# Kernel optimization log

Measured on AMD Instinct MI355X. Metric: run time of the kernel, lower is better.

## Reference

```python
import jax, jax.numpy as jnp
import numpy as np

# Grouped masked GEMM dims (see DeepSeekMOE._up_gate/_down):
# G = num_experts // ep = 8; M = m_per_group = 32
# up/gate: k = hidden_size = 4096, n = 2*expert_dim = 2816
# down   : k = expert_dim  = 1408, n = hidden_size = 4096
G, M = 8, 32
K_UG, N_UG = 4096, 2816
K_DN, N_DN = 1408, 4096


def setup_inputs() -> dict:
    key = jax.random.key(0)
    k1, k2, k3, k4, k5 = jax.random.split(key, 5)
    x_ug = jax.random.normal(k1, (G, M, K_UG), dtype=jnp.float32)
    w_ug = jax.random.normal(k2, (G, N_UG, K_UG), dtype=jnp.float32) * 0.02  # NT layout [g, n, k]
    x_dn = jax.random.normal(k3, (G, M, K_DN), dtype=jnp.float32)
    w_dn = jax.random.normal(k4, (G, N_DN, K_DN), dtype=jnp.float32) * 0.02  # NT layout [g, n, k]
    masked_m = jax.random.randint(k5, (G,), 0, M, dtype=jnp.int32)  # per-group valid row count
    return {"x_ug": x_ug, "w_ug": w_ug, "x_dn": x_dn, "w_dn": w_dn, "masked_m": masked_m}


def reference(x_ug, w_ug, x_dn, w_dn, masked_m):
    # Row-validity mask: rows >= masked_m[g] are skipped by the masked grouped GEMM
    # (their output is zero / undefined; we define it as zero).
    row = jnp.arange(M, dtype=jnp.int32)
    mask = (row[None, :] < masked_m[:, None])[:, :, None]  # [G, M, 1]

    # Masked grouped GEMM, NT layout: out[g] = x[g] @ w[g].T on valid rows.
    out_ug = jnp.einsum('gmk,gnk->gmn', x_ug, w_ug)  # [G, M, N_UG]  up/gate proj
    out_dn = jnp.einsum('gmk,gnk->gmn', x_dn, w_dn)  # [G, M, N_DN]  down proj

    out_ug = jnp.where(mask, out_ug, jnp.zeros((), out_ug.dtype))
    out_dn = jnp.where(mask, out_dn, jnp.zeros((), out_dn.dtype))
    # Pack both grouped-GEMM outputs into one array along the feature dim.
    return jnp.concatenate([out_ug, out_dn], axis=-1)  # [G, M, N_UG + N_DN]
```

## Files before the change

kernel.cpp:

```cpp
#include <hip/hip_runtime.h>
#include <hip/hip_bf16.h>


#define G_    8
#define M_    32
#define KUG   4096
#define NUG   2816
#define KDN   1408
#define NDN   4096
#define NOUT  (NUG + NDN)
#define UPT   (NUG / 32)
#define DNT   (NDN / 32)
#define UPG   (UPT + DNT)
#define BK    128

typedef __attribute__((ext_vector_type(8))) short bf16x8;
typedef __attribute__((ext_vector_type(4))) float f32x4;

typedef __attribute__((address_space(3))) float        lds_f32;
typedef const __attribute__((address_space(1))) float  gbl_f32;

__device__ __forceinline__ short f2bf(float x) {
  union { __hip_bfloat16 h; short s; } u;
  u.h = __hip_bfloat16(x);
  return u.s;
}

__device__ __forceinline__ bf16x8 cvt8(f32x4 lo, f32x4 hi) {
  bf16x8 o;
#pragma unroll
  for (int j = 0; j < 4; ++j) { o[j] = f2bf(lo[j]); o[4 + j] = f2bf(hi[j]); }
  return o;
}

__global__ __launch_bounds__(64, 2) void moe_masked_gemm(
    const float* __restrict__ x_ug, const float* __restrict__ w_ug,
    const float* __restrict__ x_dn, const float* __restrict__ w_dn,
    const int* __restrict__ masked_m, float* __restrict__ out) {
  __shared__ float wbuf[32 * BK];

  int b = blockIdx.x;
  int g = b & 7;
  int u = b >> 3;

  const float* wg;
  const float* xg;
  int K, NIT, n0, colOff;
  if (u < UPT) {
    K = KUG; NIT = KUG / BK; n0 = u * 32; colOff = 0;
    wg = w_ug + ((size_t)g * NUG + n0) * KUG;
    xg = x_ug + (size_t)g * M_ * KUG;
  } else {
    int ud = u - UPT;
    K = KDN; NIT = KDN / BK; n0 = ud * 32; colOff = NUG;
    wg = w_dn + ((size_t)g * NDN + n0) * KDN;
    xg = x_dn + (size_t)g * M_ * KDN;
  }

  int mm = masked_m[g];
  int t   = threadIdx.x;
  int r   = t & 15, q4 = t >> 4;
  int l5  = t >> 5, q32 = t & 31;
  int s   = r & 7;

  f32x4 acc00 = {0.f, 0.f, 0.f, 0.f}, acc01 = {0.f, 0.f, 0.f, 0.f};
  f32x4 acc10 = {0.f, 0.f, 0.f, 0.f}, acc11 = {0.f, 0.f, 0.f, 0.f};

  if (mm != 0) {
    for (int it = 0; it < NIT; ++it) {
      int k0 = it * BK;

#pragma unroll
      for (int i = 0; i < 16; ++i) {
        int row = 2 * i + l5;
        int qs  = q32 ^ (row & 7);
        __builtin_amdgcn_global_load_lds(
            (gbl_f32*)(wg + (size_t)row * K + k0 + qs * 4),
            (lds_f32*)(wbuf + i * 256 + t * 4), 16, 0, 0);
      }

      f32x4 xv[2][4][2];
#pragma unroll
      for (int mf = 0; mf < 2; ++mf) {
#pragma unroll
        for (int ks = 0; ks < 4; ++ks) {
          const float* xp = xg + (size_t)(mf * 16 + r) * K + k0 + ks * 32 + q4 * 8;
          xv[mf][ks][0] = *(const f32x4*)xp;
          xv[mf][ks][1] = *(const f32x4*)(xp + 4);
        }
      }

      asm volatile("s_waitcnt vmcnt(0)" ::: "memory");
      __builtin_amdgcn_sched_barrier(0);

#pragma unroll
      for (int ks = 0; ks < 4; ++ks) {
        int g0 = (ks * 4 + q4) * 2;
        const float* row0 = wbuf + (size_t)r * BK;
        const float* row1 = wbuf + (size_t)(16 + r) * BK;
        f32x4 w0a = *(const f32x4*)(row0 + (((g0)     ^ s) << 2));
        f32x4 w0b = *(const f32x4*)(row0 + (((g0 + 1) ^ s) << 2));
        f32x4 w1a = *(const f32x4*)(row1 + (((g0)     ^ s) << 2));
        f32x4 w1b = *(const f32x4*)(row1 + (((g0 + 1) ^ s) << 2));
        bf16x8 b0 = cvt8(w0a, w0b);
        bf16x8 b1 = cvt8(w1a, w1b);
        bf16x8 a0 = cvt8(xv[0][ks][0], xv[0][ks][1]);
        bf16x8 a1 = cvt8(xv[1][ks][0], xv[1][ks][1]);
        acc00 = __builtin_amdgcn_mfma_f32_16x16x32_bf16(a0, b0, acc00, 0, 0, 0);
        acc01 = __builtin_amdgcn_mfma_f32_16x16x32_bf16(a0, b1, acc01, 0, 0, 0);
        acc10 = __builtin_amdgcn_mfma_f32_16x16x32_bf16(a1, b0, acc10, 0, 0, 0);
        acc11 = __builtin_amdgcn_mfma_f32_16x16x32_bf16(a1, b1, acc11, 0, 0, 0);
      }
    }
  }

  float* outg = out + (size_t)g * M_ * NOUT + colOff + n0;
#pragma unroll
  for (int i = 0; i < 4; ++i) {
    int m0 = q4 * 4 + i;
    int m1 = 16 + m0;
    outg[(size_t)m0 * NOUT + r]      = (m0 < mm) ? acc00[i] : 0.f;
    outg[(size_t)m0 * NOUT + 16 + r] = (m0 < mm) ? acc01[i] : 0.f;
    outg[(size_t)m1 * NOUT + r]      = (m1 < mm) ? acc10[i] : 0.f;
    outg[(size_t)m1 * NOUT + 16 + r] = (m1 < mm) ? acc11[i] : 0.f;
  }
}

extern "C" void kernel_launch(void* const* d_in, const int* in_sizes, int n_in,
                              void* d_out, int out_size, void* d_ws, size_t ws_size,
                              hipStream_t stream) {
  const float* x_ug     = (const float*)d_in[0];
  const float* w_ug     = (const float*)d_in[1];
  const float* x_dn     = (const float*)d_in[2];
  const float* w_dn     = (const float*)d_in[3];
  const int*   masked_m = (const int*)d_in[4];
  float*       out      = (float*)d_out;

  moe_masked_gemm<<<dim3(G_ * UPG), dim3(64), 0, stream>>>(
      x_ug, w_ug, x_dn, w_dn, masked_m, out);
}
```

Before: 122.9 us.

## Split weight staging into two 16-row halves, use larger BK for up-proj, interleave block order

The weight tile is now staged in two 16-row halves, each computed right after it lands, so the same LDS buffer is reused. The up/gate projection uses a 256-wide K step while the down projection keeps 128, which halves the up-proj loop iteration count. Block indices are remapped so each period of 27 blocks mixes 11 up and 16 down tiles, spreading the long and short blocks evenly over the CUs. The cost is an extra serialized vmcnt wait per iteration between the halves, so there is less load/compute overlap inside a block.

```diff
diff --git a/kernel.cpp b/kernel.cpp
--- a/kernel.cpp
+++ b/kernel.cpp
@@ -12,7 +12,6 @@
 #define UPT   (NUG / 32)
 #define DNT   (NDN / 32)
 #define UPG   (UPT + DNT)
-#define BK    128
 
 typedef __attribute__((ext_vector_type(8))) short bf16x8;
 typedef __attribute__((ext_vector_type(4))) float f32x4;
@@ -33,85 +32,117 @@
   return o;
 }
 
+template<int BK>
+__device__ __forceinline__ void stage16(const float* wrows, float* wbuf,
+                                        int K, int k0, int t) {
+  constexpr int GPR = BK / 4;
+  constexpr int NI  = 16 * GPR / 64;
+#pragma unroll
+  for (int i = 0; i < NI; ++i) {
+    int gid = i * 64 + t;
+    int row = gid / GPR;
+    int q   = gid % GPR;
+    int qs  = q ^ (row & 7);
+    __builtin_amdgcn_global_load_lds(
+        (gbl_f32*)(wrows + (size_t)row * K + k0 + qs * 4),
+        (lds_f32*)(wbuf + gid * 4), 16, 0, 0);
+  }
+}
+
+template<int NKS>
+__device__ __forceinline__ void comp16(const float* wbuf, const bf16x8 (&xb)[2][NKS],
+                                       int r, int q4, int s,
+                                       f32x4& accM0, f32x4& accM1) {
+  constexpr int BK = NKS * 32;
+#pragma unroll
+  for (int ks = 0; ks < NKS; ++ks) {
+    int g0 = (ks * 4 + q4) * 2;
+    const float* rowp = wbuf + (size_t)r * BK;
+    f32x4 wlo = *(const f32x4*)(rowp + (((g0)     ^ s) << 2));
+    f32x4 whi = *(const f32x4*)(rowp + (((g0 + 1) ^ s) << 2));
+    bf16x8 bb = cvt8(wlo, whi);
+    accM0 = __builtin_amdgcn_mfma_f32_16x16x32_bf16(xb[0][ks], bb, accM0, 0, 0, 0);
+    accM1 = __builtin_amdgcn_mfma_f32_16x16x32_bf16(xb[1][ks], bb, accM1, 0, 0, 0);
+  }
+}
+
+template<int NKS, int NIT>
+__device__ __forceinline__ void run_unit(const float* wg, const float* xg,
+                                         float* wbuf, int K, int t,
+                                         f32x4& acc00, f32x4& acc01,
+                                         f32x4& acc10, f32x4& acc11) {
+  constexpr int BK = NKS * 32;
+  int r = t & 15, q4 = t >> 4, s = r & 7;
+  for (int it = 0; it < NIT; ++it) {
+    int k0 = it * BK;
+
+    stage16<BK>(wg, wbuf, K, k0, t);
+    f32x4 xv[2][NKS][2];
+#pragma unroll
+    for (int mf = 0; mf < 2; ++mf)
+#pragma unroll
+      for (int ks = 0; ks < NKS; ++ks) {
+        const float* xp = xg + (size_t)(mf * 16 + r) * K + k0 + ks * 32 + q4 * 8;
+        xv[mf][ks][0] = *(const f32x4*)xp;
+        xv[mf][ks][1] = *(const f32x4*)(xp + 4);
+      }
+    asm volatile("s_waitcnt vmcnt(0)" ::: "memory");
+    __builtin_amdgcn_sched_barrier(0);
+
+    bf16x8 xb[2][NKS];
+#pragma unroll
+    for (int mf = 0; mf < 2; ++mf)
+#pragma unroll
+      for (int ks = 0; ks < NKS; ++ks)
+        xb[mf][ks] = cvt8(xv[mf][ks][0], xv[mf][ks][1]);
+
+    comp16<NKS>(wbuf, xb, r, q4, s, acc00, acc10);
+
+    stage16<BK>(wg + (size_t)16 * K, wbuf, K, k0, t);
+    asm volatile("s_waitcnt vmcnt(0)" ::: "memory");
+    __builtin_amdgcn_sched_barrier(0);
+
+    comp16<NKS>(wbuf, xb, r, q4, s, acc01, acc11);
+  }
+}
+
 __global__ __launch_bounds__(64, 2) void moe_masked_gemm(
     const float* __restrict__ x_ug, const float* __restrict__ w_ug,
     const float* __restrict__ x_dn, const float* __restrict__ w_dn,
     const int* __restrict__ masked_m, float* __restrict__ out) {
-  __shared__ float wbuf[32 * BK];
+  __shared__ float wbuf[16 * 256];
 
   int b = blockIdx.x;
   int g = b & 7;
-  int u = b >> 3;
+  int v = b >> 3;
+  int period = v / 27, slot = v - period * 27;
+  int u = (slot < 11) ? (period * 11 + slot) : (UPT + period * 16 + (slot - 11));
 
   const float* wg;
   const float* xg;
-  int K, NIT, n0, colOff;
-  if (u < UPT) {
-    K = KUG; NIT = KUG / BK; n0 = u * 32; colOff = 0;
+  int K, n0, colOff;
+  bool is_up = (u < UPT);
+  if (is_up) {
+    K = KUG; n0 = u * 32; colOff = 0;
     wg = w_ug + ((size_t)g * NUG + n0) * KUG;
     xg = x_ug + (size_t)g * M_ * KUG;
   } else {
     int ud = u - UPT;
-    K = KDN; NIT = KDN / BK; n0 = ud * 32; colOff = NUG;
+    K = KDN; n0 = ud * 32; colOff = NUG;
     wg = w_dn + ((size_t)g * NDN + n0) * KDN;
     xg = x_dn + (size_t)g * M_ * KDN;
   }
 
   int mm = masked_m[g];
-  int t   = threadIdx.x;
-  int r   = t & 15, q4 = t >> 4;
-  int l5  = t >> 5, q32 = t & 31;
-  int s   = r & 7;
+  int t  = threadIdx.x;
+  int r  = t & 15, q4 = t >> 4;
 
   f32x4 acc00 = {0.f, 0.f, 0.f, 0.f}, acc01 = {0.f, 0.f, 0.f, 0.f};
   f32x4 acc10 = {0.f, 0.f, 0.f, 0.f}, acc11 = {0.f, 0.f, 0.f, 0.f};
 
   if (mm != 0) {
-    for (int it = 0; it < NIT; ++it) {
-      int k0 = it * BK;
-
-#pragma unroll
-      for (int i = 0; i < 16; ++i) {
-        int row = 2 * i + l5;
-        int qs  = q32 ^ (row & 7);
-        __builtin_amdgcn_global_load_lds(
-            (gbl_f32*)(wg + (size_t)row * K + k0 + qs * 4),
-            (lds_f32*)(wbuf + i * 256 + t * 4), 16, 0, 0);
-      }
-
-      f32x4 xv[2][4][2];
-#pragma unroll
-      for (int mf = 0; mf < 2; ++mf) {
-#pragma unroll
-        for (int ks = 0; ks < 4; ++ks) {
-          const float* xp = xg + (size_t)(mf * 16 + r) * K + k0 + ks * 32 + q4 * 8;
-          xv[mf][ks][0] = *(const f32x4*)xp;
-          xv[mf][ks][1] = *(const f32x4*)(xp + 4);
-        }
-      }
-
-      asm volatile("s_waitcnt vmcnt(0)" ::: "memory");
-      __builtin_amdgcn_sched_barrier(0);
-
-#pragma unroll
-      for (int ks = 0; ks < 4; ++ks) {
-        int g0 = (ks * 4 + q4) * 2;
-        const float* row0 = wbuf + (size_t)r * BK;
-        const float* row1 = wbuf + (size_t)(16 + r) * BK;
-        f32x4 w0a = *(const f32x4*)(row0 + (((g0)     ^ s) << 2));
-        f32x4 w0b = *(const f32x4*)(row0 + (((g0 + 1) ^ s) << 2));
-        f32x4 w1a = *(const f32x4*)(row1 + (((g0)     ^ s) << 2));
-        f32x4 w1b = *(const f32x4*)(row1 + (((g0 + 1) ^ s) << 2));
-        bf16x8 b0 = cvt8(w0a, w0b);
-        bf16x8 b1 = cvt8(w1a, w1b);
-        bf16x8 a0 = cvt8(xv[0][ks][0], xv[0][ks][1]);
-        bf16x8 a1 = cvt8(xv[1][ks][0], xv[1][ks][1]);
-        acc00 = __builtin_amdgcn_mfma_f32_16x16x32_bf16(a0, b0, acc00, 0, 0, 0);
-        acc01 = __builtin_amdgcn_mfma_f32_16x16x32_bf16(a0, b1, acc01, 0, 0, 0);
-        acc10 = __builtin_amdgcn_mfma_f32_16x16x32_bf16(a1, b0, acc10, 0, 0, 0);
-        acc11 = __builtin_amdgcn_mfma_f32_16x16x32_bf16(a1, b1, acc11, 0, 0, 0);
-      }
-    }
+    if (is_up) run_unit<8, KUG / 256>(wg, xg, wbuf, K, t, acc00, acc01, acc10, acc11);
+    else       run_unit<4, KDN / 128>(wg, xg, wbuf, K, t, acc00, acc01, acc10, acc11);
   }
 
   float* outg = out + (size_t)g * M_ * NOUT + colOff + n0;
```

New measurement: 142.5 us. 1.16x slower.

## Widen N tile to 64, pre-convert activations to bf16, interleave up/down blocks

Applied to the files above, without the earlier changes.

Doubles the per-block N tile from 32 to 64 columns so each activation fragment feeds four MFMA column tiles, halving the activation reloads per weight column. Adds two small pre-pass kernels that convert x_ug and x_dn to bf16 in workspace, so the GEMM reads half the activation bytes and skips per-iteration conversion. Reorders the block index so up and down tiles are interleaved in an 11:16 ratio to balance their differing K lengths across the grid. The cost is fewer blocks (half the grid), a doubled LDS tile that may lower occupancy, and two extra launches.

```diff
diff --git a/kernel.cpp b/kernel.cpp
--- a/kernel.cpp
+++ b/kernel.cpp
@@ -9,10 +9,14 @@
 #define KDN   1408
 #define NDN   4096
 #define NOUT  (NUG + NDN)
-#define UPT   (NUG / 32)
-#define DNT   (NDN / 32)
+#define BN    64
+#define BK    128
+#define UPT   (NUG / BN)
+#define DNT   (NDN / BN)
 #define UPG   (UPT + DNT)
-#define BK    128
+#define XUG_E (G_ * M_ * KUG)
+#define XDN_E (G_ * M_ * KDN)
+#define XBF_BYTES ((size_t)(XUG_E + XDN_E) * 2)
 
 typedef __attribute__((ext_vector_type(8))) short bf16x8;
 typedef __attribute__((ext_vector_type(4))) float f32x4;
@@ -33,61 +37,91 @@
   return o;
 }
 
+__global__ void cvt_x_kernel(const float* __restrict__ src, short* __restrict__ dst,
+                             int n8) {
+  int i = blockIdx.x * 256 + threadIdx.x;
+  if (i < n8) {
+    f32x4 lo = *(const f32x4*)(src + (size_t)i * 8);
+    f32x4 hi = *(const f32x4*)(src + (size_t)i * 8 + 4);
+    *(bf16x8*)(dst + (size_t)i * 8) = cvt8(lo, hi);
+  }
+}
+
+template<bool XBF>
 __global__ __launch_bounds__(64, 2) void moe_masked_gemm(
     const float* __restrict__ x_ug, const float* __restrict__ w_ug,
     const float* __restrict__ x_dn, const float* __restrict__ w_dn,
+    const short* __restrict__ xbf_ug, const short* __restrict__ xbf_dn,
     const int* __restrict__ masked_m, float* __restrict__ out) {
-  __shared__ float wbuf[32 * BK];
+  __shared__ float wbuf[BN * BK];
 
   int b = blockIdx.x;
   int g = b & 7;
-  int u = b >> 3;
+  int v = b >> 3;
+  int p = v / 27, s = v - p * 27;
+  int ub = (s * 11 + 16) / 27;
+  bool is_up = ((s * 11) % 27) < 11;
 
   const float* wg;
-  const float* xg;
-  int K, NIT, n0, colOff;
-  if (u < UPT) {
-    K = KUG; NIT = KUG / BK; n0 = u * 32; colOff = 0;
+  const float* xf;
+  const short* xq;
+  int K, n0, colOff, NIT;
+  if (is_up) {
+    int u = p * 11 + ub;
+    K = KUG; NIT = KUG / BK; n0 = u * BN; colOff = 0;
     wg = w_ug + ((size_t)g * NUG + n0) * KUG;
-    xg = x_ug + (size_t)g * M_ * KUG;
+    xf = x_ug + (size_t)g * M_ * KUG;
+    xq = xbf_ug + (size_t)g * M_ * KUG;
   } else {
-    int ud = u - UPT;
-    K = KDN; NIT = KDN / BK; n0 = ud * 32; colOff = NUG;
+    int d = p * 16 + (s - ub);
+    K = KDN; NIT = KDN / BK; n0 = d * BN; colOff = NUG;
     wg = w_dn + ((size_t)g * NDN + n0) * KDN;
-    xg = x_dn + (size_t)g * M_ * KDN;
+    xf = x_dn + (size_t)g * M_ * KDN;
+    xq = xbf_dn + (size_t)g * M_ * KDN;
   }
 
   int mm = masked_m[g];
-  int t   = threadIdx.x;
-  int r   = t & 15, q4 = t >> 4;
-  int l5  = t >> 5, q32 = t & 31;
-  int s   = r & 7;
+  int t  = threadIdx.x;
+  int r  = t & 15, q4 = t >> 4;
+  int sk = r & 7;
 
-  f32x4 acc00 = {0.f, 0.f, 0.f, 0.f}, acc01 = {0.f, 0.f, 0.f, 0.f};
-  f32x4 acc10 = {0.f, 0.f, 0.f, 0.f}, acc11 = {0.f, 0.f, 0.f, 0.f};
+  f32x4 acc[2][4];
+#pragma unroll
+  for (int mf = 0; mf < 2; ++mf)
+#pragma unroll
+    for (int nf = 0; nf < 4; ++nf) acc[mf][nf] = (f32x4){0.f, 0.f, 0.f, 0.f};
 
   if (mm != 0) {
     for (int it = 0; it < NIT; ++it) {
       int k0 = it * BK;
 
 #pragma unroll
-      for (int i = 0; i < 16; ++i) {
-        int row = 2 * i + l5;
-        int qs  = q32 ^ (row & 7);
+      for (int i = 0; i < 32; ++i) {
+        int gid = i * 64 + t;
+        int row = gid >> 5;
+        int q   = gid & 31;
+        int qs  = q ^ (row & 7);
         __builtin_amdgcn_global_load_lds(
             (gbl_f32*)(wg + (size_t)row * K + k0 + qs * 4),
-            (lds_f32*)(wbuf + i * 256 + t * 4), 16, 0, 0);
+            (lds_f32*)(wbuf + gid * 4), 16, 0, 0);
       }
 
-      f32x4 xv[2][4][2];
+      bf16x8 xb[2][4];
+      if constexpr (XBF) {
 #pragma unroll
-      for (int mf = 0; mf < 2; ++mf) {
+        for (int mf = 0; mf < 2; ++mf)
 #pragma unroll
-        for (int ks = 0; ks < 4; ++ks) {
-          const float* xp = xg + (size_t)(mf * 16 + r) * K + k0 + ks * 32 + q4 * 8;
-          xv[mf][ks][0] = *(const f32x4*)xp;
-          xv[mf][ks][1] = *(const f32x4*)(xp + 4);
-        }
+          for (int ks = 0; ks < 4; ++ks)
+            xb[mf][ks] = *(const bf16x8*)(xq + (size_t)(mf * 16 + r) * K +
+                                          k0 + ks * 32 + q4 * 8);
+      } else {
+#pragma unroll
+        for (int mf = 0; mf < 2; ++mf)
+#pragma unroll
+          for (int ks = 0; ks < 4; ++ks) {
+            const float* xp = xf + (size_t)(mf * 16 + r) * K + k0 + ks * 32 + q4 * 8;
+            xb[mf][ks] = cvt8(*(const f32x4*)xp, *(const f32x4*)(xp + 4));
+          }
       }
 
       asm volatile("s_waitcnt vmcnt(0)" ::: "memory");
@@ -96,20 +130,14 @@
 #pragma unroll
       for (int ks = 0; ks < 4; ++ks) {
         int g0 = (ks * 4 + q4) * 2;
-        const float* row0 = wbuf + (size_t)r * BK;
-        const float* row1 = wbuf + (size_t)(16 + r) * BK;
-        f32x4 w0a = *(const f32x4*)(row0 + (((g0)     ^ s) << 2));
-        f32x4 w0b = *(const f32x4*)(row0 + (((g0 + 1) ^ s) << 2));
-        f32x4 w1a = *(const f32x4*)(row1 + (((g0)     ^ s) << 2));
-        f32x4 w1b = *(const f32x4*)(row1 + (((g0 + 1) ^ s) << 2));
-        bf16x8 b0 = cvt8(w0a, w0b);
-        bf16x8 b1 = cvt8(w1a, w1b);
-        bf16x8 a0 = cvt8(xv[0][ks][0], xv[0][ks][1]);
-        bf16x8 a1 = cvt8(xv[1][ks][0], xv[1][ks][1]);
-        acc00 = __builtin_amdgcn_mfma_f32_16x16x32_bf16(a0, b0, acc00, 0, 0, 0);
-        acc01 = __builtin_amdgcn_mfma_f32_16x16x32_bf16(a0, b1, acc01, 0, 0, 0);
-        acc10 = __builtin_amdgcn_mfma_f32_16x16x32_bf16(a1, b0, acc10, 0, 0, 0);
-        acc11 = __builtin_amdgcn_mfma_f32_16x16x32_bf16(a1, b1, acc11, 0, 0, 0);
+        int o0 = ((g0 ^ sk) << 2), o1 = (((g0 + 1) ^ sk) << 2);
+#pragma unroll
+        for (int nf = 0; nf < 4; ++nf) {
+          const float* rowp = wbuf + (size_t)(nf * 16 + r) * BK;
+          bf16x8 bb = cvt8(*(const f32x4*)(rowp + o0), *(const f32x4*)(rowp + o1));
+          acc[0][nf] = __builtin_amdgcn_mfma_f32_16x16x32_bf16(xb[0][ks], bb, acc[0][nf], 0, 0, 0);
+          acc[1][nf] = __builtin_amdgcn_mfma_f32_16x16x32_bf16(xb[1][ks], bb, acc[1][nf], 0, 0, 0);
+        }
       }
     }
   }
@@ -117,12 +145,13 @@
   float* outg = out + (size_t)g * M_ * NOUT + colOff + n0;
 #pragma unroll
   for (int i = 0; i < 4; ++i) {
-    int m0 = q4 * 4 + i;
-    int m1 = 16 + m0;
-    outg[(size_t)m0 * NOUT + r]      = (m0 < mm) ? acc00[i] : 0.f;
-    outg[(size_t)m0 * NOUT + 16 + r] = (m0 < mm) ? acc01[i] : 0.f;
-    outg[(size_t)m1 * NOUT + r]      = (m1 < mm) ? acc10[i] : 0.f;
-    outg[(size_t)m1 * NOUT + 16 + r] = (m1 < mm) ? acc11[i] : 0.f;
+    int m0 = q4 * 4 + i, m1 = 16 + m0;
+    bool v0 = m0 < mm, v1 = m1 < mm;
+#pragma unroll
+    for (int nf = 0; nf < 4; ++nf) {
+      outg[(size_t)m0 * NOUT + nf * 16 + r] = v0 ? acc[0][nf][i] : 0.f;
+      outg[(size_t)m1 * NOUT + nf * 16 + r] = v1 ? acc[1][nf][i] : 0.f;
+    }
   }
 }
 
@@ -136,6 +165,16 @@
   const int*   masked_m = (const int*)d_in[4];
   float*       out      = (float*)d_out;
 
-  moe_masked_gemm<<<dim3(G_ * UPG), dim3(64), 0, stream>>>(
-      x_ug, w_ug, x_dn, w_dn, masked_m, out);
+  short* xbf_ug = (short*)d_ws;
+  short* xbf_dn = xbf_ug + XUG_E;
+
+  if (ws_size >= XBF_BYTES) {
+    cvt_x_kernel<<<dim3(XUG_E / 8 / 256), dim3(256), 0, stream>>>(x_ug, xbf_ug, XUG_E / 8);
+    cvt_x_kernel<<<dim3(XDN_E / 8 / 256), dim3(256), 0, stream>>>(x_dn, xbf_dn, XDN_E / 8);
+    moe_masked_gemm<true><<<dim3(G_ * UPG), dim3(64), 0, stream>>>(
+        x_ug, w_ug, x_dn, w_dn, xbf_ug, xbf_dn, masked_m, out);
+  } else {
+    moe_masked_gemm<false><<<dim3(G_ * UPG), dim3(64), 0, stream>>>(
+        x_ug, w_ug, x_dn, w_dn, xbf_ug, xbf_dn, masked_m, out);
+  }
 }
```

After: 137.0 us. +11.5%, slower.
